# Optimization experiments

Measured on AMD Instinct MI355X. Metric: run time of the kernel, lower is better.

The kernel has to match this reference:

```python
import jax, jax.numpy as jnp
import numpy as np

VOCAB, E, HIDDEN = 100000, 64, (64, 128, 64)
B, T = 4096, 200


def setup_inputs() -> dict:
    key = jax.random.key(0)
    ks = jax.random.split(key, 12)
    # glorot-ish scales
    def glorot(k, shape):
        fan_in, fan_out = shape[0], shape[-1]
        s = jnp.sqrt(6.0 / (fan_in + fan_out))
        return jax.random.uniform(k, shape, jnp.float32, -s, s)
    return {
        "query": jax.random.randint(ks[0], (B,), 0, VOCAB),
        "keys": jax.random.randint(ks[1], (B, T), 0, VOCAB),
        "emb": glorot(ks[2], (VOCAB, E)),
        "att_w1": glorot(ks[3], (4 * E, 64)),
        "att_b1": jnp.zeros((64,), jnp.float32),
        "att_w2": glorot(ks[4], (64, 1)),
        "att_b2": jnp.zeros((1,), jnp.float32),
        "deep_w1": glorot(ks[5], (HIDDEN[0], HIDDEN[1])),
        "deep_b1": jnp.zeros((HIDDEN[1],), jnp.float32),
        "deep_w2": glorot(ks[6], (HIDDEN[1], HIDDEN[2])),
        "deep_b2": jnp.zeros((HIDDEN[2],), jnp.float32),
        "out_w": glorot(ks[7], (HIDDEN[2], 1)),
        "out_b": jnp.zeros((1,), jnp.float32),
    }


def reference(query, keys, emb, att_w1, att_b1, att_w2, att_b2,
              deep_w1, deep_b1, deep_w2, deep_b2, out_w, out_b):
    q = emb[query]                # [B, E]
    k = emb[keys]                 # [B, T, E]
    qe = jnp.broadcast_to(q[:, None, :], k.shape)  # [B, T, E]
    inter = jnp.concatenate([qe, k, qe - k, qe * k], axis=-1)  # [B, T, 4E]
    h = jax.nn.relu(inter @ att_w1 + att_b1)       # [B, T, 64]
    scores = (h @ att_w2 + att_b2)[..., 0]         # [B, T]
    w = jax.nn.softmax(scores, axis=-1)            # [B, T]
    interest = jnp.einsum("bt,bte->be", w, k)      # [B, E]
    d = jax.nn.relu(interest @ deep_w1 + deep_b1)
    d = jax.nn.relu(d @ deep_w2 + deep_b2)
    return jax.nn.sigmoid(d @ out_w + out_b)       # [B, 1]
```

## Files before the change

### kernel.cpp

```cpp
#include <hip/hip_runtime.h>

#define T 200
#define E 64
#define TPAD 256
#define ROW 72
#define BDIM 256

typedef __bf16 bf16_t;
typedef __bf16 bf16x8 __attribute__((ext_vector_type(8)));
typedef float f32x4 __attribute__((ext_vector_type(4)));

__global__ __launch_bounds__(256) void pre_cvt(const float* __restrict__ embf,
                                               bf16_t* __restrict__ emb16, int n8,
                                               const float* __restrict__ w1,
                                               float* __restrict__ Ap,
                                               float* __restrict__ Ctf,
                                               float* __restrict__ Dtf) {
    const int bid = blockIdx.x;
    if (bid < 16) {
        const int idx = bid * 256 + threadIdx.x;
        const int e = idx >> 6, j = idx & 63;
        const float a = w1[e * 64 + j];
        const float b = w1[(64 + e) * 64 + j];
        const float c = w1[(128 + e) * 64 + j];
        const float d = w1[(192 + e) * 64 + j];
        Ap[e * 64 + j]  = a + c;
        Ctf[j * 64 + e] = b - c;
        Dtf[j * 64 + e] = d;
        return;
    }
    const int i = (bid - 16) * 256 + threadIdx.x;
    if (i >= n8) return;
    const float4* s = (const float4*)embf + (size_t)i * 2;
    const float4 a = s[0], b = s[1];
    union { bf16_t h[8]; uint4 v; } u;
    u.h[0] = (bf16_t)a.x; u.h[1] = (bf16_t)a.y; u.h[2] = (bf16_t)a.z; u.h[3] = (bf16_t)a.w;
    u.h[4] = (bf16_t)b.x; u.h[5] = (bf16_t)b.y; u.h[6] = (bf16_t)b.z; u.h[7] = (bf16_t)b.w;
    ((uint4*)emb16)[i] = u.v;
}

__global__ __launch_bounds__(256, 2) void din_wave(
    const int* __restrict__ query,
    const int* __restrict__ keys,
    const bf16_t* __restrict__ emb16,
    const float* __restrict__ Ap,
    const float* __restrict__ Ctf,
    const float* __restrict__ Dtf,
    const float* __restrict__ b1,
    const float* __restrict__ w2,
    const float* __restrict__ b2,
    const float* __restrict__ dw1,
    const float* __restrict__ db1,
    const float* __restrict__ dw2,
    const float* __restrict__ db2,
    const float* __restrict__ ow,
    const float* __restrict__ ob,
    float* __restrict__ out,
    const int nB)
{
    __shared__ __align__(16) char smem[4 * 1664];
    const int tid  = threadIdx.x;
    const int wid  = tid >> 6;
    const int lane = tid & 63;
    const int n    = lane & 15;
    const int quad = lane >> 4;
    const int b    = blockIdx.x * 4 + wid;
    if (b >= nB) return;

    float* sWgt = (float*)(smem + wid * 1664);
    float* sInt = (float*)(smem + wid * 1664 + 832);
    float* sD1  = (float*)(smem + wid * 1664 + 1088);

    const int qi = query[b];
    const bf16x8 q0 = *(const bf16x8*)(emb16 + (size_t)qi * E + quad * 8);
    const bf16x8 q1 = *(const bf16x8*)(emb16 + (size_t)qi * E + 32 + quad * 8);

    int kidx[13];
    #pragma unroll
    for (int mt = 0; mt < 13; ++mt) {
        const int t = mt * 16 + n;
        kidx[mt] = (t < T) ? keys[b * T + t] : 0;
    }
    bf16x8 a0[13], a1[13];
    #pragma unroll
    for (int mt = 0; mt < 13; ++mt) {
        const bf16_t* rp = emb16 + (size_t)kidx[mt] * E;
        a0[mt] = *(const bf16x8*)(rp + quad * 8);
        a1[mt] = *(const bf16x8*)(rp + 32 + quad * 8);
    }

    float u = 0.f;
    #pragma unroll
    for (int e = 0; e < 64; ++e)
        u = fmaf((float)emb16[(size_t)qi * E + e], Ap[e * 64 + lane], u);

    float uv[4], w2v[4];
    #pragma unroll
    for (int nt = 0; nt < 4; ++nt) {
        const int jj = nt * 16 + n;
        uv[nt]  = b1[jj] + __shfl(u, jj);
        w2v[nt] = w2[jj];
    }

    bf16x8 bF[4][2];
    #pragma unroll
    for (int nt = 0; nt < 4; ++nt) {
        const int jj = nt * 16 + n;
        const float* cb = Ctf + jj * 64;
        const float* db = Dtf + jj * 64;
        union { bf16_t h[8]; bf16x8 v; } u0, u1;
        #pragma unroll
        for (int x = 0; x < 8; ++x) {
            u0.h[x] = (bf16_t)fmaf((float)q0[x], db[quad * 8 + x],      cb[quad * 8 + x]);
            u1.h[x] = (bf16_t)fmaf((float)q1[x], db[32 + quad * 8 + x], cb[32 + quad * 8 + x]);
        }
        bF[nt][0] = u0.v;
        bF[nt][1] = u1.v;
    }

    #pragma unroll
    for (int mt = 0; mt < 13; ++mt) {
        float s0 = 0.f, s1 = 0.f, s2 = 0.f, s3 = 0.f;
        #pragma unroll
        for (int nt = 0; nt < 4; ++nt) {
            f32x4 acc = { uv[nt], uv[nt], uv[nt], uv[nt] };
            acc = __builtin_amdgcn_mfma_f32_16x16x32_bf16(a0[mt], bF[nt][0], acc, 0, 0, 0);
            acc = __builtin_amdgcn_mfma_f32_16x16x32_bf16(a1[mt], bF[nt][1], acc, 0, 0, 0);
            s0 = fmaf(fmaxf(acc[0], 0.f), w2v[nt], s0);
            s1 = fmaf(fmaxf(acc[1], 0.f), w2v[nt], s1);
            s2 = fmaf(fmaxf(acc[2], 0.f), w2v[nt], s2);
            s3 = fmaf(fmaxf(acc[3], 0.f), w2v[nt], s3);
        }
        #pragma unroll
        for (int off = 1; off < 16; off <<= 1) {
            s0 += __shfl_xor(s0, off);
            s1 += __shfl_xor(s1, off);
            s2 += __shfl_xor(s2, off);
            s3 += __shfl_xor(s3, off);
        }
        if (n == 0) {
            const int base = mt * 16 + quad * 4;
            sWgt[base + 0] = s0;
            sWgt[base + 1] = s1;
            sWgt[base + 2] = s2;
            sWgt[base + 3] = s3;
        }
    }
    asm volatile("s_waitcnt lgkmcnt(0)" ::: "memory");
    __builtin_amdgcn_sched_barrier(0);

    {
        const float b2v = b2[0];
        const float x0 = sWgt[lane] + b2v;
        const float x1 = sWgt[64 + lane] + b2v;
        const float x2 = sWgt[128 + lane] + b2v;
        const float x3 = (lane < 8) ? (sWgt[192 + lane] + b2v) : -1e30f;
        float m = fmaxf(fmaxf(x0, x1), fmaxf(x2, x3));
        #pragma unroll
        for (int off = 32; off > 0; off >>= 1) m = fmaxf(m, __shfl_xor(m, off));
        const float p0 = __expf(x0 - m);
        const float p1 = __expf(x1 - m);
        const float p2 = __expf(x2 - m);
        const float p3 = (lane < 8) ? __expf(x3 - m) : 0.f;
        float s = ((p0 + p1) + (p2 + p3));
        #pragma unroll
        for (int off = 32; off > 0; off >>= 1) s += __shfl_xor(s, off);
        const float inv = 1.f / s;
        sWgt[lane]       = p0 * inv;
        sWgt[64 + lane]  = p1 * inv;
        sWgt[128 + lane] = p2 * inv;
        if (lane < 8) sWgt[192 + lane] = p3 * inv;
    }
    asm volatile("s_waitcnt lgkmcnt(0)" ::: "memory");
    __builtin_amdgcn_sched_barrier(0);

    {
        float pa[8], pb[8];
        #pragma unroll
        for (int x = 0; x < 8; ++x) { pa[x] = 0.f; pb[x] = 0.f; }
        #pragma unroll
        for (int mt = 0; mt < 13; ++mt) {
            const int t = mt * 16 + n;
            const float wt = (t < T) ? sWgt[t] : 0.f;
            #pragma unroll
            for (int x = 0; x < 8; ++x) {
                pa[x] = fmaf(wt, (float)a0[mt][x], pa[x]);
                pb[x] = fmaf(wt, (float)a1[mt][x], pb[x]);
            }
        }
        #pragma unroll
        for (int x = 0; x < 8; ++x) {
            #pragma unroll
            for (int off = 1; off < 16; off <<= 1) {
                pa[x] += __shfl_xor(pa[x], off);
                pb[x] += __shfl_xor(pb[x], off);
            }
        }
        if (n == 0) {
            #pragma unroll
            for (int x = 0; x < 8; ++x) {
                sInt[quad * 8 + x]      = pa[x];
                sInt[32 + quad * 8 + x] = pb[x];
            }
        }
    }
    asm volatile("s_waitcnt lgkmcnt(0)" ::: "memory");
    __builtin_amdgcn_sched_barrier(0);

    {
        float d1a = db1[lane], d1b = db1[64 + lane];
        #pragma unroll
        for (int e = 0; e < 64; ++e) {
            const float ie = sInt[e];
            d1a = fmaf(ie, dw1[e * 128 + lane], d1a);
            d1b = fmaf(ie, dw1[e * 128 + 64 + lane], d1b);
        }
        sD1[lane]      = fmaxf(d1a, 0.f);
        sD1[64 + lane] = fmaxf(d1b, 0.f);
    }
    asm volatile("s_waitcnt lgkmcnt(0)" ::: "memory");
    __builtin_amdgcn_sched_barrier(0);

    {
        float o = db2[lane];
        #pragma unroll
        for (int i = 0; i < 128; ++i)
            o = fmaf(sD1[i], dw2[i * 64 + lane], o);
        float v = fmaxf(o, 0.f) * ow[lane];
        #pragma unroll
        for (int off = 32; off > 0; off >>= 1) v += __shfl_xor(v, off);
        if (lane == 0) out[b] = 1.f / (1.f + __expf(-(v + ob[0])));
    }
}

__global__ __launch_bounds__(BDIM, 3) void din_kernel(
    const int* __restrict__ query,
    const int* __restrict__ keys,
    const float* __restrict__ embf,
    const bf16_t* __restrict__ emb16,
    const int use16,
    const float* __restrict__ w1,
    const float* __restrict__ b1,
    const float* __restrict__ w2,
    const float* __restrict__ b2,
    const float* __restrict__ dw1,
    const float* __restrict__ db1,
    const float* __restrict__ dw2,
    const float* __restrict__ db2,
    const float* __restrict__ ow,
    const float* __restrict__ ob,
    float* __restrict__ out)
{
    __shared__ __align__(16) char sRaw[TPAD * ROW * 2];
    __shared__ __align__(16) bf16_t sMt[64 * ROW];
    __shared__ float sU[64];
    __shared__ float sUP[256];
    __shared__ float sW2f[64];
    __shared__ float sWgt[256];
    __shared__ float sQf[64];
    __shared__ __align__(16) char sQtmp[128];
    __shared__ float sRed[8];
    __shared__ float sInt[64];
    __shared__ float sD1[128];
    __shared__ float sD2[64];

    const int tid  = threadIdx.x;
    const int lane = tid & 63;
    const int wid  = tid >> 6;
    const int b    = blockIdx.x;
    const float b2v = b2[0];

    uint4 kr[8];
    if (tid < T) {
        const int ki = keys[b * T + tid];
        if (use16) {
            const uint4* kp = (const uint4*)(emb16 + (size_t)ki * E);
            #pragma unroll
            for (int c = 0; c < 8; ++c) kr[c] = kp[c];
        } else {
            const float4* kp = (const float4*)(embf + (size_t)ki * E);
            #pragma unroll
            for (int c = 0; c < 8; ++c) {
                const float4 x = kp[2 * c], y = kp[2 * c + 1];
                union { bf16_t h[8]; uint4 v; } u;
                u.h[0] = (bf16_t)x.x; u.h[1] = (bf16_t)x.y; u.h[2] = (bf16_t)x.z; u.h[3] = (bf16_t)x.w;
                u.h[4] = (bf16_t)y.x; u.h[5] = (bf16_t)y.y; u.h[6] = (bf16_t)y.z; u.h[7] = (bf16_t)y.w;
                kr[c] = u.v;
            }
        }
    } else {
        #pragma unroll
        for (int c = 0; c < 8; ++c) kr[c] = make_uint4(0u, 0u, 0u, 0u);
    }

    const int qi = query[b];
    if (tid < 8) {
        uint4 qv;
        if (use16) {
            qv = ((const uint4*)(emb16 + (size_t)qi * E))[tid];
        } else {
            const float4 x = ((const float4*)(embf + (size_t)qi * E))[2 * tid];
            const float4 y = ((const float4*)(embf + (size_t)qi * E))[2 * tid + 1];
            union { bf16_t h[8]; uint4 v; } u;
            u.h[0] = (bf16_t)x.x; u.h[1] = (bf16_t)x.y; u.h[2] = (bf16_t)x.z; u.h[3] = (bf16_t)x.w;
            u.h[4] = (bf16_t)y.x; u.h[5] = (bf16_t)y.y; u.h[6] = (bf16_t)y.z; u.h[7] = (bf16_t)y.w;
            qv = u.v;
        }
        ((uint4*)sQtmp)[tid] = qv;
    }
    if (tid < 64) sW2f[tid] = w2[tid];
    __syncthreads();
    if (tid < 64) sQf[tid] = (float)((const bf16_t*)sQtmp)[tid];
    __syncthreads();

    {
        float* sTmp = (float*)sRaw;
        const int j = tid & 63, ec = tid >> 6;
        float au = 0.f;
        #pragma unroll
        for (int eo = 0; eo < 16; ++eo) {
            const int e = ec * 16 + eo;
            const float w1a = w1[e * 64 + j];
            const float w1b = w1[(64 + e) * 64 + j];
            const float w1c = w1[(128 + e) * 64 + j];
            const float w1d = w1[(192 + e) * 64 + j];
            sTmp[e * 65 + j] = w1b - w1c + sQf[e] * w1d;
            au = fmaf(sQf[e], w1a + w1c, au);
        }
        sUP[tid] = au;
    }
    __syncthreads();
    {
        const float* sTmp = (const float*)sRaw;
        const int e = tid & 63, jc = tid >> 6;
        #pragma unroll
        for (int jo = 0; jo < 16; ++jo) {
            const int j = jc * 16 + jo;
            sMt[j * ROW + e] = (bf16_t)sTmp[e * 65 + j];
        }
    }
    if (tid < 64) sU[tid] = b1[tid] + sUP[tid] + sUP[64 + tid] + sUP[128 + tid] + sUP[192 + tid];
    __syncthreads();

    bf16_t* sK = (bf16_t*)sRaw;
    {
        uint4* dst = (uint4*)(sK + tid * ROW);
        #pragma unroll
        for (int c = 0; c < 8; ++c) dst[c] = kr[c];
    }
    __syncthreads();

    {
        const int n    = lane & 15;
        const int quad = lane >> 4;
        float w2v[4], uv[4];
        bf16x8 bF[4][2];
        #pragma unroll
        for (int nt = 0; nt < 4; ++nt) {
            w2v[nt] = sW2f[nt * 16 + n];
            uv[nt]  = sU[nt * 16 + n];
            bF[nt][0] = *(const bf16x8*)&sMt[(nt * 16 + n) * ROW + quad * 8];
            bF[nt][1] = *(const bf16x8*)&sMt[(nt * 16 + n) * ROW + 32 + quad * 8];
        }
        #pragma unroll
        for (int i = 0; i < 4; ++i) {
            const int mt = wid * 4 + i;
            const bf16x8 a0 = *(const bf16x8*)&sK[(mt * 16 + n) * ROW + quad * 8];
            const bf16x8 a1 = *(const bf16x8*)&sK[(mt * 16 + n) * ROW + 32 + quad * 8];
            float s0 = 0.f, s1 = 0.f, s2 = 0.f, s3 = 0.f;
            #pragma unroll
            for (int nt = 0; nt < 4; ++nt) {
                f32x4 acc = { uv[nt], uv[nt], uv[nt], uv[nt] };
                acc = __builtin_amdgcn_mfma_f32_16x16x32_bf16(a0, bF[nt][0], acc, 0, 0, 0);
                acc = __builtin_amdgcn_mfma_f32_16x16x32_bf16(a1, bF[nt][1], acc, 0, 0, 0);
                s0 = fmaf(fmaxf(acc[0], 0.f), w2v[nt], s0);
                s1 = fmaf(fmaxf(acc[1], 0.f), w2v[nt], s1);
                s2 = fmaf(fmaxf(acc[2], 0.f), w2v[nt], s2);
                s3 = fmaf(fmaxf(acc[3], 0.f), w2v[nt], s3);
            }
            #pragma unroll
            for (int off = 1; off < 16; off <<= 1) {
                s0 += __shfl_xor(s0, off);
                s1 += __shfl_xor(s1, off);
                s2 += __shfl_xor(s2, off);
                s3 += __shfl_xor(s3, off);
            }
            if (n == 0) {
                const int base = mt * 16 + quad * 4;
                sWgt[base + 0] = s0;
                sWgt[base + 1] = s1;
                sWgt[base + 2] = s2;
                sWgt[base + 3] = s3;
            }
        }
    }
    __syncthreads();

    {
        const float score = (tid < T) ? (sWgt[tid] + b2v) : -1e30f;
        float m = score;
        #pragma unroll
        for (int off = 32; off > 0; off >>= 1) m = fmaxf(m, __shfl_xor(m, off));
        if (lane == 0) sRed[wid] = m;
        __syncthreads();
        const float gmax = fmaxf(fmaxf(sRed[0], sRed[1]), fmaxf(sRed[2], sRed[3]));
        const float p = (tid < T) ? __expf(score - gmax) : 0.f;
        float s = p;
        #pragma unroll
        for (int off = 32; off > 0; off >>= 1) s += __shfl_xor(s, off);
        if (lane == 0) sRed[4 + wid] = s;
        __syncthreads();
        const float gsum = sRed[4] + sRed[5] + sRed[6] + sRed[7];
        sWgt[tid] = p / gsum;
    }
    __syncthreads();

    {
        const int e = tid & 63, ch = tid >> 6;
        float a = 0.f;
        #pragma unroll 8
        for (int tt = 0; tt < 64; ++tt) {
            const int t = ch * 64 + tt;
            a = fmaf(sWgt[t], (float)sK[t * ROW + e], a);
        }
        sUP[tid] = a;
    }
    __syncthreads();
    if (tid < 64) sInt[tid] = sUP[tid] + sUP[64 + tid] + sUP[128 + tid] + sUP[192 + tid];
    __syncthreads();

    if (tid < 128) {
        float a = db1[tid];
        #pragma unroll 8
        for (int e = 0; e < 64; ++e) a = fmaf(sInt[e], dw1[e * 128 + tid], a);
        sD1[tid] = fmaxf(a, 0.f);
    }
    __syncthreads();
    if (tid < 64) {
        float a = db2[tid];
        #pragma unroll 8
        for (int i = 0; i < 128; ++i) a = fmaf(sD1[i], dw2[i * 64 + tid], a);
        sD2[tid] = fmaxf(a, 0.f);
    }
    __syncthreads();
    if (tid < 64) {
        float v = sD2[tid] * ow[tid];
        #pragma unroll
        for (int off = 32; off > 0; off >>= 1) v += __shfl_xor(v, off);
        if (tid == 0) out[b] = 1.f / (1.f + __expf(-(v + ob[0])));
    }
}

extern "C" void kernel_launch(void* const* d_in, const int* in_sizes, int n_in,
                              void* d_out, int out_size, void* d_ws, size_t ws_size,
                              hipStream_t stream) {
    const int*   query = (const int*)d_in[0];
    const int*   keys  = (const int*)d_in[1];
    const float* embf  = (const float*)d_in[2];
    const float* w1    = (const float*)d_in[3];
    const float* b1    = (const float*)d_in[4];
    const float* w2    = (const float*)d_in[5];
    const float* b2    = (const float*)d_in[6];
    const float* dw1   = (const float*)d_in[7];
    const float* db1   = (const float*)d_in[8];
    const float* dw2   = (const float*)d_in[9];
    const float* db2   = (const float*)d_in[10];
    const float* ow    = (const float*)d_in[11];
    const float* ob    = (const float*)d_in[12];
    float* out = (float*)d_out;
    const int B        = in_sizes[0];
    const int embElems = in_sizes[2];
    const size_t WOFF  = 49152;

    if (ws_size >= WOFF + (size_t)embElems * 2) {
        float*  Ap    = (float*)d_ws;
        float*  Ctf   = (float*)((char*)d_ws + 16384);
        float*  Dtf   = (float*)((char*)d_ws + 32768);
        bf16_t* emb16 = (bf16_t*)((char*)d_ws + WOFF);
        const int n8 = embElems / 8;
        pre_cvt<<<16 + (n8 + 255) / 256, 256, 0, stream>>>(embf, emb16, n8,
                                                           w1, Ap, Ctf, Dtf);
        din_wave<<<(B + 3) / 4, BDIM, 0, stream>>>(query, keys, emb16, Ap, Ctf, Dtf,
                                                   b1, w2, b2, dw1, db1, dw2, db2,
                                                   ow, ob, out, B);
    } else {
        din_kernel<<<B, BDIM, 0, stream>>>(query, keys, embf, (const bf16_t*)d_ws, 0,
                                           w1, b1, w2, b2, dw1, db1, dw2, db2, ow, ob, out);
    }
}
```

Baseline: 145.8 us.

## Launch one wavefront per batch row and split FMA chains into parallel accumulators

The per-row kernel now runs as 64-thread blocks, one per batch element, with launch bounds of (64, 4), instead of 256-thread blocks holding four independent wavefronts. The query projection and the two dense MLP layers now use several partial accumulators in place of one serial fmaf chain, which shortens dependency latency. The smaller blocks give the scheduler finer-grained work but change the occupancy hint and may shift register allocation. The multi-accumulator sums also reorder the floating-point additions slightly.

```diff
diff --git a/kernel.cpp b/kernel.cpp
--- a/kernel.cpp
+++ b/kernel.cpp
@@ -39,7 +39,7 @@
     ((uint4*)emb16)[i] = u.v;
 }
 
-__global__ __launch_bounds__(256, 2) void din_wave(
+__global__ __launch_bounds__(64, 4) void din_wave(
     const int* __restrict__ query,
     const int* __restrict__ keys,
     const bf16_t* __restrict__ emb16,
@@ -58,18 +58,16 @@
     float* __restrict__ out,
     const int nB)
 {
-    __shared__ __align__(16) char smem[4 * 1664];
-    const int tid  = threadIdx.x;
-    const int wid  = tid >> 6;
-    const int lane = tid & 63;
+    __shared__ __align__(16) char smem[1664];
+    const int lane = threadIdx.x;
     const int n    = lane & 15;
     const int quad = lane >> 4;
-    const int b    = blockIdx.x * 4 + wid;
+    const int b    = blockIdx.x;
     if (b >= nB) return;
 
-    float* sWgt = (float*)(smem + wid * 1664);
-    float* sInt = (float*)(smem + wid * 1664 + 832);
-    float* sD1  = (float*)(smem + wid * 1664 + 1088);
+    float* sWgt = (float*)smem;
+    float* sInt = (float*)(smem + 832);
+    float* sD1  = (float*)(smem + 1088);
 
     const int qi = query[b];
     const bf16x8 q0 = *(const bf16x8*)(emb16 + (size_t)qi * E + quad * 8);
@@ -89,10 +87,15 @@
         a1[mt] = *(const bf16x8*)(rp + 32 + quad * 8);
     }
 
-    float u = 0.f;
+    float ua = 0.f, ub = 0.f, uc = 0.f, ud = 0.f;
     #pragma unroll
-    for (int e = 0; e < 64; ++e)
-        u = fmaf((float)emb16[(size_t)qi * E + e], Ap[e * 64 + lane], u);
+    for (int e = 0; e < 64; e += 4) {
+        ua = fmaf((float)emb16[(size_t)qi * E + e],     Ap[e * 64 + lane],       ua);
+        ub = fmaf((float)emb16[(size_t)qi * E + e + 1], Ap[(e + 1) * 64 + lane], ub);
+        uc = fmaf((float)emb16[(size_t)qi * E + e + 2], Ap[(e + 2) * 64 + lane], uc);
+        ud = fmaf((float)emb16[(size_t)qi * E + e + 3], Ap[(e + 3) * 64 + lane], ud);
+    }
+    const float u = (ua + ub) + (uc + ud);
 
     float uv[4], w2v[4];
     #pragma unroll
@@ -208,25 +211,32 @@
     __builtin_amdgcn_sched_barrier(0);
 
     {
-        float d1a = db1[lane], d1b = db1[64 + lane];
-        #pragma unroll
-        for (int e = 0; e < 64; ++e) {
-            const float ie = sInt[e];
-            d1a = fmaf(ie, dw1[e * 128 + lane], d1a);
-            d1b = fmaf(ie, dw1[e * 128 + 64 + lane], d1b);
-        }
-        sD1[lane]      = fmaxf(d1a, 0.f);
-        sD1[64 + lane] = fmaxf(d1b, 0.f);
+        float d1a0 = db1[lane], d1a1 = 0.f;
+        float d1b0 = db1[64 + lane], d1b1 = 0.f;
+        #pragma unroll
+        for (int e = 0; e < 64; e += 2) {
+            const float ie0 = sInt[e], ie1 = sInt[e + 1];
+            d1a0 = fmaf(ie0, dw1[e * 128 + lane], d1a0);
+            d1a1 = fmaf(ie1, dw1[(e + 1) * 128 + lane], d1a1);
+            d1b0 = fmaf(ie0, dw1[e * 128 + 64 + lane], d1b0);
+            d1b1 = fmaf(ie1, dw1[(e + 1) * 128 + 64 + lane], d1b1);
+        }
+        sD1[lane]      = fmaxf(d1a0 + d1a1, 0.f);
+        sD1[64 + lane] = fmaxf(d1b0 + d1b1, 0.f);
     }
     asm volatile("s_waitcnt lgkmcnt(0)" ::: "memory");
     __builtin_amdgcn_sched_barrier(0);
 
     {
-        float o = db2[lane];
-        #pragma unroll
-        for (int i = 0; i < 128; ++i)
-            o = fmaf(sD1[i], dw2[i * 64 + lane], o);
-        float v = fmaxf(o, 0.f) * ow[lane];
+        float o0 = db2[lane], o1 = 0.f, o2 = 0.f, o3 = 0.f;
+        #pragma unroll
+        for (int i = 0; i < 128; i += 4) {
+            o0 = fmaf(sD1[i],     dw2[i * 64 + lane],       o0);
+            o1 = fmaf(sD1[i + 1], dw2[(i + 1) * 64 + lane], o1);
+            o2 = fmaf(sD1[i + 2], dw2[(i + 2) * 64 + lane], o2);
+            o3 = fmaf(sD1[i + 3], dw2[(i + 3) * 64 + lane], o3);
+        }
+        float v = fmaxf((o0 + o1) + (o2 + o3), 0.f) * ow[lane];
         #pragma unroll
         for (int off = 32; off > 0; off >>= 1) v += __shfl_xor(v, off);
         if (lane == 0) out[b] = 1.f / (1.f + __expf(-(v + ob[0])));
@@ -480,9 +490,9 @@
         const int n8 = embElems / 8;
         pre_cvt<<<16 + (n8 + 255) / 256, 256, 0, stream>>>(embf, emb16, n8,
                                                            w1, Ap, Ctf, Dtf);
-        din_wave<<<(B + 3) / 4, BDIM, 0, stream>>>(query, keys, emb16, Ap, Ctf, Dtf,
-                                                   b1, w2, b2, dw1, db1, dw2, db2,
-                                                   ow, ob, out, B);
+        din_wave<<<B, 64, 0, stream>>>(query, keys, emb16, Ap, Ctf, Dtf,
+                                       b1, w2, b2, dw1, db1, dw2, db2,
+                                       ow, ob, out, B);
     } else {
         din_kernel<<<B, BDIM, 0, stream>>>(query, keys, embf, (const bf16_t*)d_ws, 0,
                                            w1, b1, w2, b2, dw1, db1, dw2, db2, ow, ob, out);
```

Result: slower. 182.3 us (+25.0%).
